# Optimization experiments

Hardware: AMD Instinct MI355X
Metric: run time of the kernel (lower is better)

The kernel has to match this reference:

```python
import jax, jax.numpy as jnp
import numpy as np

TEMP = 0.3
EPS = 1e-09
EPS2 = 1e-10


def _unit(v):
    return v / jnp.linalg.norm(v, axis=-1, keepdims=True)


def setup_inputs() -> dict:
    key = jax.random.key(0)
    k1, k2 = jax.random.split(key)
    T, Q, D, K = 512, 8, 64, 16  # tracks, queries/track, embed dim, detections/track
    x = _unit(jax.random.normal(k1, (T * K, D), dtype=jnp.float32))
    y = _unit(jax.random.normal(k2, (T, Q, D), dtype=jnp.float32))
    track_idxs = jnp.repeat(jnp.arange(T, dtype=jnp.int64), K)  # every track id present
    return {"x": x, "track_idxs": track_idxs, "y": y}


def reference(x, track_idxs, y):
    # local_contrast=True, separate_tracks=False, static_contrast=False,
    # use_hard_condition=False, shift_to_positive=False (module defaults).
    T, Q, D = y.shape
    # All track ids 0..T-1 appear in track_idxs (by construction), so
    # ut_ids = unique(track_idxs) = arange(T) and y[ut_ids] = y.
    ut_ids = jnp.arange(T, dtype=track_idxs.dtype)
    y_flat = y.reshape(T * Q, D)          # flatten(0,1)
    y_idxs = jnp.tile(ut_ids, Q)          # ut_ids.repeat(Q) in torch semantics
    # Pairwise exp-scaled similarities: [N, T*Q]
    S = jnp.exp(jnp.einsum("nd,md->nm", x, y_flat) / TEMP)
    # Positive pairs: same track id (each x row belongs to exactly one uid),
    # so the per-uid loop collapses to one masked reduction.
    M = track_idxs[:, None] == y_idxs[None, :]
    num = jnp.sum(jnp.where(M, S, 0.0))
    den = jnp.sum(jnp.where(M, 0.0, S))
    loss = -jnp.log(num / (den + num + EPS) + EPS2)
    return loss.reshape(1)
```

## Files before the change

### kernel.cpp

```cpp
#include <hip/hip_runtime.h>
#include <hip/hip_bf16.h>

#define NROWS 8192
#define MROWS 4096
#define DDIM  64
#define TNUM  512
#define BTM   128
#define BTN   128
#define MT    2
#define GXM   (NROWS / BTM)
#define GYM   (MROWS / (BTN * MT))
#define NBLK_MAIN (GXM * GYM)
#define NPART (NBLK_MAIN * 4)
#define EXP2_SCALE 4.8089834696298780f

using bf16x8 = __attribute__((ext_vector_type(8))) short;
using f32x4  = __attribute__((ext_vector_type(4))) float;

__device__ __forceinline__ float fast_exp2(float f) {
    return __builtin_amdgcn_exp2f(f);
}
__device__ __forceinline__ short f2bf(float f) {
    __hip_bfloat16 h = __float2bfloat16(f);
    short s; __builtin_memcpy(&s, &h, 2); return s;
}

__device__ __forceinline__ int swz(int row, int colbyte) {
    return ((row << 7) + colbyte) ^ ((row & 7) << 4);
}

template <bool SCALE>
__device__ __forceinline__ void stage_tile(const float4* __restrict__ src,
                                           short* __restrict__ dst, int t) {
    #pragma unroll
    for (int q = 0; q < 8; ++q) {
        const int g = q * 256 + t;
        const int row = g >> 4, c4 = g & 15;
        float4 v = src[g];
        short4 o;
        if (SCALE) {
            o.x = f2bf(v.x * EXP2_SCALE); o.y = f2bf(v.y * EXP2_SCALE);
            o.z = f2bf(v.z * EXP2_SCALE); o.w = f2bf(v.w * EXP2_SCALE);
        } else {
            o.x = f2bf(v.x); o.y = f2bf(v.y); o.z = f2bf(v.z); o.w = f2bf(v.w);
        }
        *(short4*)((char*)dst + swz(row, c4 << 3)) = o;
    }
}

extern "C" __global__ __launch_bounds__(256)
void ContrastiveLoss_56435870269983_kernel(
    const float* __restrict__ x, const float* __restrict__ y,
    const int* __restrict__ tid_raw,
    float2* __restrict__ part)
{
    __shared__ short xs[BTM * DDIM];
    __shared__ short ys[BTN * DDIM];

    const int t    = threadIdx.x;
    const int lane = t & 63;
    const int wave = t >> 6;
    const int bid  = blockIdx.x;
    const int bx   = bid & (GXM - 1);
    const int byg  = bid >> 6;

    const int n0blk  = bx * BTM;
    const int m0base = byg * (BTN * MT);

    const int n0   = (wave >> 1) * 64;
    const int m0w  = (wave & 1) * 64;
    const int rsel = lane & 15;
    const int kb   = (lane >> 4) << 4;

    const bool is64 = (tid_raw[17] != 1);
    int tia[4][4];
    #pragma unroll
    for (int i = 0; i < 4; ++i) {
        const int base = n0blk + n0 + i * 16 + (lane >> 4) * 4;
        if (!is64) {
            int4 v = *(const int4*)(tid_raw + base);
            tia[i][0] = v.x; tia[i][1] = v.y; tia[i][2] = v.z; tia[i][3] = v.w;
        } else {
            #pragma unroll
            for (int r = 0; r < 4; ++r) tia[i][r] = tid_raw[2 * (base + r)];
        }
    }

    stage_tile<true >((const float4*)(x + (size_t)n0blk * DDIM), xs, t);
    stage_tile<false>((const float4*)(y + (size_t)m0base * DDIM), ys, t);
    __syncthreads();

    float sa4[4] = {0.f, 0.f, 0.f, 0.f};
    float sp2[2] = {0.f, 0.f};

    #pragma unroll
    for (int mt = 0; mt < MT; ++mt) {
        f32x4 acc[4][4];
        #pragma unroll
        for (int i = 0; i < 4; ++i)
            #pragma unroll
            for (int j = 0; j < 4; ++j) acc[i][j] = (f32x4){0.f, 0.f, 0.f, 0.f};

        #pragma unroll
        for (int s = 0; s < 2; ++s) {
            bf16x8 af[4], bfr[4];
            #pragma unroll
            for (int i = 0; i < 4; ++i)
                af[i] = *(const bf16x8*)((const char*)xs + swz(n0 + i * 16 + rsel, kb + s * 64));
            #pragma unroll
            for (int j = 0; j < 4; ++j)
                bfr[j] = *(const bf16x8*)((const char*)ys + swz(m0w + j * 16 + rsel, kb + s * 64));
            #pragma unroll
            for (int i = 0; i < 4; ++i)
                #pragma unroll
                for (int j = 0; j < 4; ++j)
                    acc[i][j] = __builtin_amdgcn_mfma_f32_16x16x32_bf16(
                        af[i], bfr[j], acc[i][j], 0, 0, 0);
        }
        __syncthreads();

        if (mt + 1 < MT)
            stage_tile<false>((const float4*)(y + (size_t)(m0base + (mt + 1) * BTN) * DDIM), ys, t);

        const int mrow = m0base + mt * BTN + m0w;
        int yc[4];
        #pragma unroll
        for (int j = 0; j < 4; ++j) yc[j] = (mrow + j * 16 + rsel) & (TNUM - 1);
        #pragma unroll
        for (int i = 0; i < 4; ++i)
            #pragma unroll
            for (int j = 0; j < 4; ++j)
                #pragma unroll
                for (int r = 0; r < 4; ++r) {
                    float e = fast_exp2(acc[i][j][r]);
                    sa4[r] += e;
                    if (tia[i][r] == yc[j]) sp2[r & 1] += e;
                }

        if (mt + 1 < MT) __syncthreads();
    }

    float sa = (sa4[0] + sa4[1]) + (sa4[2] + sa4[3]);
    float sp = sp2[0] + sp2[1];

    #pragma unroll
    for (int off = 32; off; off >>= 1) {
        sa += __shfl_down(sa, off, 64);
        sp += __shfl_down(sp, off, 64);
    }
    if (lane == 0) part[bid * 4 + wave] = make_float2(sa, sp);
}

extern "C" __global__ __launch_bounds__(256)
void cl_final_v10(const float2* __restrict__ part, unsigned int* __restrict__ out)
{
    __shared__ float red[2][256];
    const int t = threadIdx.x;
    float a = 0.0f, p = 0.0f;
    #pragma unroll
    for (int i = t; i < NPART; i += 256) {
        float2 v = part[i];
        a += v.x; p += v.y;
    }
    red[0][t] = a; red[1][t] = p;
    __syncthreads();
    for (int s = 128; s > 0; s >>= 1) {
        if (t < s) { red[0][t] += red[0][t + s]; red[1][t] += red[1][t + s]; }
        __syncthreads();
    }
    if (t == 0) {
        float total = red[0][0];
        float num   = red[1][0];
        float loss  = -__logf(num / (total + 1e-9f) + 1e-10f);
        __hip_bfloat16 bh = __float2bfloat16(loss);
        unsigned short h; __builtin_memcpy(&h, &bh, 2);
        out[0] = ((unsigned int)h << 16) | (unsigned int)h;
    }
}

extern "C" void kernel_launch(void* const* d_in, const int* in_sizes, int n_in,
                              void* d_out, int out_size, void* d_ws, size_t ws_size,
                              hipStream_t stream) {
    const float* x   = (const float*)d_in[0];
    const int*   tid = (const int*)d_in[1];
    const float* y   = (const float*)d_in[2];

    float2* part = (float2*)d_ws;
    ContrastiveLoss_56435870269983_kernel<<<NBLK_MAIN, 256, 0, stream>>>(
        x, y, tid, part);
    cl_final_v10<<<1, 256, 0, stream>>>(part, (unsigned int*)d_out);
}
```

Before: 22.21 us.

## Double-buffer y tiles in LDS with register prefetch and smaller N tile

Splits the y tile into 64-row chunks across four iterations and keeps two LDS buffers. The next chunk's global loads are issued into registers before the MFMA and exp work on the current chunk, then converted and written to the other buffer, which removes one barrier per iteration. A launch-bounds occupancy hint of 4 is also added. Each wave now issues fewer MFMAs per LDS fragment load, and the extra prefetch registers may limit occupancy.

```diff
diff --git a/kernel.cpp b/kernel.cpp
--- a/kernel.cpp
+++ b/kernel.cpp
@@ -6,8 +6,8 @@
 #define DDIM  64
 #define TNUM  512
 #define BTM   128
-#define BTN   128
-#define MT    2
+#define BTN   64
+#define MT    4
 #define GXM   (NROWS / BTM)
 #define GYM   (MROWS / (BTN * MT))
 #define NBLK_MAIN (GXM * GYM)
@@ -29,33 +29,15 @@
     return ((row << 7) + colbyte) ^ ((row & 7) << 4);
 }
 
-template <bool SCALE>
-__device__ __forceinline__ void stage_tile(const float4* __restrict__ src,
-                                           short* __restrict__ dst, int t) {
-    #pragma unroll
-    for (int q = 0; q < 8; ++q) {
-        const int g = q * 256 + t;
-        const int row = g >> 4, c4 = g & 15;
-        float4 v = src[g];
-        short4 o;
-        if (SCALE) {
-            o.x = f2bf(v.x * EXP2_SCALE); o.y = f2bf(v.y * EXP2_SCALE);
-            o.z = f2bf(v.z * EXP2_SCALE); o.w = f2bf(v.w * EXP2_SCALE);
-        } else {
-            o.x = f2bf(v.x); o.y = f2bf(v.y); o.z = f2bf(v.z); o.w = f2bf(v.w);
-        }
-        *(short4*)((char*)dst + swz(row, c4 << 3)) = o;
-    }
-}
-
-extern "C" __global__ __launch_bounds__(256)
+extern "C" __global__ __launch_bounds__(256, 4)
 void ContrastiveLoss_56435870269983_kernel(
     const float* __restrict__ x, const float* __restrict__ y,
     const int* __restrict__ tid_raw,
     float2* __restrict__ part)
 {
     __shared__ short xs[BTM * DDIM];
-    __shared__ short ys[BTN * DDIM];
+    __shared__ short ys0[BTN * DDIM];
+    __shared__ short ys1[BTN * DDIM];
 
     const int t    = threadIdx.x;
     const int lane = t & 63;
@@ -68,7 +50,7 @@
     const int m0base = byg * (BTN * MT);
 
     const int n0   = (wave >> 1) * 64;
-    const int m0w  = (wave & 1) * 64;
+    const int m0w  = (wave & 1) * 32;
     const int rsel = lane & 15;
     const int kb   = (lane >> 4) << 4;
 
@@ -86,8 +68,31 @@
         }
     }
 
-    stage_tile<true >((const float4*)(x + (size_t)n0blk * DDIM), xs, t);
-    stage_tile<false>((const float4*)(y + (size_t)m0base * DDIM), ys, t);
+    {
+        const float4* xsrc = (const float4*)(x + (size_t)n0blk * DDIM);
+        #pragma unroll
+        for (int q = 0; q < 8; ++q) {
+            const int g = q * 256 + t;
+            const int row = g >> 4, c4 = g & 15;
+            float4 v = xsrc[g];
+            short4 o;
+            o.x = f2bf(v.x * EXP2_SCALE); o.y = f2bf(v.y * EXP2_SCALE);
+            o.z = f2bf(v.z * EXP2_SCALE); o.w = f2bf(v.w * EXP2_SCALE);
+            *(short4*)((char*)xs + swz(row, c4 << 3)) = o;
+        }
+    }
+    {
+        const float4* ysrc = (const float4*)(y + (size_t)m0base * DDIM);
+        #pragma unroll
+        for (int q = 0; q < 4; ++q) {
+            const int g = q * 256 + t;
+            const int row = g >> 4, c4 = g & 15;
+            float4 v = ysrc[g];
+            short4 o;
+            o.x = f2bf(v.x); o.y = f2bf(v.y); o.z = f2bf(v.z); o.w = f2bf(v.w);
+            *(short4*)((char*)ys0 + swz(row, c4 << 3)) = o;
+        }
+    }
     __syncthreads();
 
     float sa4[4] = {0.f, 0.f, 0.f, 0.f};
@@ -95,41 +100,50 @@
 
     #pragma unroll
     for (int mt = 0; mt < MT; ++mt) {
-        f32x4 acc[4][4];
+        short* cur = (mt & 1) ? ys1 : ys0;
+        short* nxt = (mt & 1) ? ys0 : ys1;
+
+        float4 st[4];
+        if (mt + 1 < MT) {
+            const float4* ysrc =
+                (const float4*)(y + (size_t)(m0base + (mt + 1) * BTN) * DDIM);
+            #pragma unroll
+            for (int q = 0; q < 4; ++q) st[q] = ysrc[q * 256 + t];
+        }
+
+        f32x4 acc[4][2];
         #pragma unroll
         for (int i = 0; i < 4; ++i)
             #pragma unroll
-            for (int j = 0; j < 4; ++j) acc[i][j] = (f32x4){0.f, 0.f, 0.f, 0.f};
+            for (int j = 0; j < 2; ++j) acc[i][j] = (f32x4){0.f, 0.f, 0.f, 0.f};
 
         #pragma unroll
         for (int s = 0; s < 2; ++s) {
-            bf16x8 af[4], bfr[4];
+            bf16x8 af[4], bfr[2];
             #pragma unroll
             for (int i = 0; i < 4; ++i)
-                af[i] = *(const bf16x8*)((const char*)xs + swz(n0 + i * 16 + rsel, kb + s * 64));
-            #pragma unroll
-            for (int j = 0; j < 4; ++j)
-                bfr[j] = *(const bf16x8*)((const char*)ys + swz(m0w + j * 16 + rsel, kb + s * 64));
+                af[i] = *(const bf16x8*)((const char*)xs +
+                        swz(n0 + i * 16 + rsel, kb + s * 64));
+            #pragma unroll
+            for (int j = 0; j < 2; ++j)
+                bfr[j] = *(const bf16x8*)((const char*)cur +
+                         swz(m0w + j * 16 + rsel, kb + s * 64));
             #pragma unroll
             for (int i = 0; i < 4; ++i)
                 #pragma unroll
-                for (int j = 0; j < 4; ++j)
+                for (int j = 0; j < 2; ++j)
                     acc[i][j] = __builtin_amdgcn_mfma_f32_16x16x32_bf16(
                         af[i], bfr[j], acc[i][j], 0, 0, 0);
         }
-        __syncthreads();
-
-        if (mt + 1 < MT)
-            stage_tile<false>((const float4*)(y + (size_t)(m0base + (mt + 1) * BTN) * DDIM), ys, t);
 
         const int mrow = m0base + mt * BTN + m0w;
-        int yc[4];
-        #pragma unroll
-        for (int j = 0; j < 4; ++j) yc[j] = (mrow + j * 16 + rsel) & (TNUM - 1);
+        int yc[2];
+        #pragma unroll
+        for (int j = 0; j < 2; ++j) yc[j] = (mrow + j * 16 + rsel) & (TNUM - 1);
         #pragma unroll
         for (int i = 0; i < 4; ++i)
             #pragma unroll
-            for (int j = 0; j < 4; ++j)
+            for (int j = 0; j < 2; ++j)
                 #pragma unroll
                 for (int r = 0; r < 4; ++r) {
                     float e = fast_exp2(acc[i][j][r]);
@@ -137,7 +151,18 @@
                     if (tia[i][r] == yc[j]) sp2[r & 1] += e;
                 }
 
-        if (mt + 1 < MT) __syncthreads();
+        if (mt + 1 < MT) {
+            #pragma unroll
+            for (int q = 0; q < 4; ++q) {
+                const int g = q * 256 + t;
+                const int row = g >> 4, c4 = g & 15;
+                short4 o;
+                o.x = f2bf(st[q].x); o.y = f2bf(st[q].y);
+                o.z = f2bf(st[q].z); o.w = f2bf(st[q].w);
+                *(short4*)((char*)nxt + swz(row, c4 << 3)) = o;
+            }
+            __syncthreads();
+        }
     }
 
     float sa = (sa4[0] + sa4[1]) + (sa4[2] + sa4[3]);
@@ -152,7 +177,7 @@
 }
 
 extern "C" __global__ __launch_bounds__(256)
-void cl_final_v10(const float2* __restrict__ part, unsigned int* __restrict__ out)
+void cl_final_v11(const float2* __restrict__ part, unsigned int* __restrict__ out)
 {
     __shared__ float red[2][256];
     const int t = threadIdx.x;
@@ -188,5 +213,5 @@
     float2* part = (float2*)d_ws;
     ContrastiveLoss_56435870269983_kernel<<<NBLK_MAIN, 256, 0, stream>>>(
         x, y, tid, part);
-    cl_final_v10<<<1, 256, 0, stream>>>(part, (unsigned int*)d_out);
-}
+    cl_final_v11<<<1, 256, 0, stream>>>(part, (unsigned int*)d_out);
+}
```

Measured after the change: 20.47 us. -7.8%, faster.
